# Optimization experiments

Hardware: AMD Instinct MI355X
Metric: run time of the kernel (lower is better)

Reference implementation:

```python
import jax, jax.numpy as jnp
import numpy as np

B, L, D, H, C = 16, 1024, 2048, 512, 2  # batch, doc_len, input_dim, hidden_dim, num_labels


def setup_inputs() -> dict:
    key = jax.random.key(0)
    ks = jax.random.split(key, 8)
    s_ih = 1.0 / np.sqrt(H)
    inp = {
        "x": jax.random.normal(ks[0], (B, L, D), dtype=jnp.float32),
        # PyTorch LSTM params (single layer, gate order i,f,g,o)
        "W_ih": jax.random.uniform(ks[1], (4 * H, D), minval=-s_ih, maxval=s_ih, dtype=jnp.float32),
        "W_hh": jax.random.uniform(ks[2], (4 * H, H), minval=-s_ih, maxval=s_ih, dtype=jnp.float32),
        "b_ih": jax.random.uniform(ks[3], (4 * H,), minval=-s_ih, maxval=s_ih, dtype=jnp.float32),
        "b_hh": jax.random.uniform(ks[4], (4 * H,), minval=-s_ih, maxval=s_ih, dtype=jnp.float32),
        # classifier linear
        "W_lin": jax.random.normal(ks[5], (C, H), dtype=jnp.float32) * 0.02,
        "b_lin": jnp.zeros((C,), dtype=jnp.float32),
        # attention gates, initialized as in the torch module
        "fwd_att": jnp.full((1, H), 0.001, dtype=jnp.float32),
        "bwd_att": jnp.full((1, H), 0.001, dtype=jnp.float32),
    }
    return inp


def _lstm(x, W_ih, W_hh, b_ih, b_hh):
    # x: [B, L, D] -> lstm_out: [B, L, H]
    b = b_ih + b_hh
    xg = jnp.einsum("bld,gd->blg", x, W_ih) + b  # precompute input projection [B,L,4H]

    def step(carry, xg_t):
        h, c = carry
        gates = xg_t + h @ W_hh.T
        i, f, g, o = jnp.split(gates, 4, axis=-1)
        i, f, o = jax.nn.sigmoid(i), jax.nn.sigmoid(f), jax.nn.sigmoid(o)
        g = jnp.tanh(g)
        c = f * c + i * g
        h = o * jnp.tanh(c)
        return (h, c), h

    h0 = jnp.zeros((x.shape[0], W_hh.shape[1]), dtype=x.dtype)
    _, hs = jax.lax.scan(step, (h0, h0), jnp.swapaxes(xg, 0, 1))
    return jnp.swapaxes(hs, 0, 1)  # [B, L, H]


def reference(x, W_ih, W_hh, b_ih, b_hh, W_lin, b_lin, fwd_att, bwd_att):
    lstm_out = _lstm(x, W_ih, W_hh, b_ih, b_hh)  # [B, L, H]
    # per-position gate: argmax of the linear classifier (same for fwd and bwd sums)
    logits = jnp.einsum("blh,ch->blc", lstm_out, W_lin) + b_lin  # [B, L, C]
    g = jnp.argmax(logits, axis=-1).astype(lstm_out.dtype)[..., None]  # [B, L, 1]
    term_f = g * lstm_out * fwd_att  # [B, L, H]
    term_b = g * lstm_out * bwd_att
    # forward_sum[i] = sum_{j<i} term_f[j]  (exclusive prefix sum)
    inc_f = jnp.cumsum(term_f, axis=1)
    cum_f = inc_f - term_f
    # backward_sum[i] = sum_{j>i} term_b[j]  (exclusive suffix sum)
    inc_b = jnp.cumsum(term_b, axis=1)
    cum_b = inc_b[:, -1:, :] - inc_b
    # fused = (lstm_out + cum_f) + (lstm_out + cum_b)
    return 2.0 * lstm_out + cum_f + cum_b
```

## Files before the change

### kernel.cpp

```cpp
#include <hip/hip_runtime.h>
#include <stdint.h>

typedef __bf16 bf16x8_t __attribute__((ext_vector_type(8)));
typedef float  f32x4_t  __attribute__((ext_vector_type(4)));

#define MFMA_BF16(A, Bv, C) __builtin_amdgcn_mfma_f32_16x16x32_bf16((A), (Bv), (C), 0, 0, 0)

static constexpr int BB = 16;
static constexpr int LL = 1024;
static constexpr int DD = 2048;
static constexpr int HH = 512;
static constexpr int GG = 4 * HH;
static constexpr int MM = BB * LL;

static constexpr size_t XBF_OFF   = 0;
static constexpr size_t WIHBF_OFF = XBF_OFF   + (size_t)MM * DD * 2;
static constexpr size_t WHHBF_OFF = WIHBF_OFF + (size_t)GG * DD * 2;
static constexpr size_t XGBF_OFF  = WHHBF_OFF + (size_t)GG * HH * 2;
static constexpr size_t GARR_OFF  = XGBF_OFF  + (size_t)MM * GG * 2;
static constexpr size_t PART_OFF  = GARR_OFF  + (size_t)MM * 4;
static constexpr size_t TBUF_OFF  = PART_OFF  + (size_t)BB * 8 * HH * 4;
static constexpr size_t WS_NEED   = TBUF_OFF  + (size_t)2 * BB * HH * 4;

__device__ __forceinline__ unsigned short f2bf(float f) {
  union { float f; uint32_t u; } v; v.f = f;
  uint32_t r = v.u + 0x7FFFu + ((v.u >> 16) & 1u);
  return (unsigned short)(r >> 16);
}
__device__ __forceinline__ float bf2f(unsigned short s) {
  union { uint32_t u; float f; } v; v.u = ((uint32_t)s) << 16;
  return v.f;
}
__device__ __forceinline__ float sigmoidf_fast(float x) { return 1.f / (1.f + __expf(-x)); }
__device__ __forceinline__ float tanhf_fast(float x) {
  float ax = fabsf(x);
  float e  = __expf(2.f * ax);
  float t  = 1.f - 2.f / (e + 1.f);
  return copysignf(t, x);
}
__device__ __forceinline__ void async_cp16(const void* g, void* lds) {
  __builtin_amdgcn_global_load_lds((const __attribute__((address_space(1))) uint32_t*)g,
                                   (__attribute__((address_space(3))) uint32_t*)lds, 16, 0, 0);
}

__global__ __launch_bounds__(256) void k_f32_to_bf16(const float* __restrict__ s,
                                                     unsigned short* __restrict__ d, int n4) {
  int i = blockIdx.x * 256 + threadIdx.x;
  int stride = gridDim.x * 256;
  for (; i < n4; i += stride) {
    float4 v = ((const float4*)s)[i];
    ushort4 o;
    o.x = f2bf(v.x); o.y = f2bf(v.y); o.z = f2bf(v.z); o.w = f2bf(v.w);
    ((ushort4*)d)[i] = o;
  }
}

__global__ __launch_bounds__(256) void k_gemm_xg(const unsigned short* __restrict__ A,
                                                 const unsigned short* __restrict__ Bw,
                                                 const float* __restrict__ b_ih,
                                                 const float* __restrict__ b_hh,
                                                 unsigned short* __restrict__ C) {
  __shared__ __align__(16) unsigned short As[128 * 32];
  __shared__ __align__(16) unsigned short Bs[128 * 32];
  const int bid = blockIdx.x;
  const int bn = bid & 15, bm = bid >> 4;
  const int row0 = bm * 128, col0 = bn * 128;
  const int tid = threadIdx.x;
  const int lane = tid & 63, w = tid >> 6;
  const int wr = w >> 1, wc = w & 1;
  const int l15 = lane & 15, l4 = lane >> 4;

  const f32x4_t z4 = {0.f, 0.f, 0.f, 0.f};
  f32x4_t acc[4][4];
#pragma unroll
  for (int mi = 0; mi < 4; ++mi)
#pragma unroll
    for (int ni = 0; ni < 4; ++ni) acc[mi][ni] = z4;

  const unsigned short* ga = A  + (size_t)(row0 + (tid >> 2)) * DD + (tid & 3) * 8;
  const unsigned short* gb = Bw + (size_t)(col0 + (tid >> 2)) * DD + (tid & 3) * 8;
  unsigned short* asw = As + w * 512;
  unsigned short* bsw = Bs + w * 512;

  for (int k0 = 0; k0 < DD; k0 += 32) {
    async_cp16(ga + k0,           asw);
    async_cp16(ga + k0 + 64 * DD, asw + 2048);
    async_cp16(gb + k0,           bsw);
    async_cp16(gb + k0 + 64 * DD, bsw + 2048);
    __syncthreads();
    bf16x8_t af[4], bfr[4];
#pragma unroll
    for (int mi = 0; mi < 4; ++mi)
      af[mi] = *(const bf16x8_t*)(As + (wr * 64 + mi * 16 + l15) * 32 + l4 * 8);
#pragma unroll
    for (int ni = 0; ni < 4; ++ni)
      bfr[ni] = *(const bf16x8_t*)(Bs + (wc * 64 + ni * 16 + l15) * 32 + l4 * 8);
#pragma unroll
    for (int mi = 0; mi < 4; ++mi)
#pragma unroll
      for (int ni = 0; ni < 4; ++ni)
        acc[mi][ni] = MFMA_BF16(af[mi], bfr[ni], acc[mi][ni]);
    __syncthreads();
  }
#pragma unroll
  for (int ni = 0; ni < 4; ++ni) {
    int col = col0 + wc * 64 + ni * 16 + l15;
    float bias = b_ih[col] + b_hh[col];
#pragma unroll
    for (int mi = 0; mi < 4; ++mi) {
      int rowb = row0 + wr * 64 + mi * 16 + l4 * 4;
#pragma unroll
      for (int r = 0; r < 4; ++r)
        C[(size_t)(rowb + r) * GG + col] = f2bf(acc[mi][ni][r] + bias);
    }
  }
}

__global__ __launch_bounds__(256) void k_lstm(const unsigned short* __restrict__ Whh,
                                              const unsigned short* __restrict__ xg,
                                              float* __restrict__ h_all,
                                              unsigned int* tbuf) {
  const int bid = blockIdx.x;
  const int b  = (bid & 7) + 8 * (bid >> 7);
  const int wg = (bid >> 3) & 15;
  const int tid = threadIdx.x;
  const int lane = tid & 63, w = tid >> 6;
  const int l15 = lane & 15, l4 = lane >> 4;
  const int K0 = wg * 32;

  __shared__ float gl[4][32];
  __shared__ __align__(16) unsigned short h_lds[HH];

  bf16x8_t wf[2][16];
#pragma unroll
  for (int mi = 0; mi < 2; ++mi) {
    const unsigned short* wrow = Whh + (size_t)(w * HH + K0 + mi * 16 + l15) * HH + l4 * 8;
#pragma unroll
    for (int kt = 0; kt < 16; ++kt)
      wf[mi][kt] = *(const bf16x8_t*)(wrow + kt * 32);
  }

  float c_reg = 0.f;
  const f32x4_t z4 = {0.f, 0.f, 0.f, 0.f};

  float xgi = 0.f, xgf = 0.f, xgc = 0.f, xgo = 0.f;
  const unsigned short* xr0 = xg + (size_t)(b << 10) * GG + K0 + (tid & 31);
  if (tid < 32) {
    xgi = bf2f(xr0[0]); xgf = bf2f(xr0[512]); xgc = bf2f(xr0[1024]); xgo = bf2f(xr0[1536]);
  }

  for (int t = 0; t < LL; ++t) {
    unsigned long long* src = (unsigned long long*)(tbuf + (((t & 1) * BB + b) << 9)) + tid;
    const unsigned int tg = (unsigned int)t;
    unsigned long long v;
    unsigned int guard = 0;
    for (;;) {
      v = __hip_atomic_load(src, __ATOMIC_RELAXED, __HIP_MEMORY_SCOPE_AGENT);
      if ((((unsigned int)(v >> 16) & 0xFFFFu) == tg) && ((unsigned int)(v >> 48) == tg)) break;
      if (++guard > (1u << 20)) break;
    }
    ushort2 hv2; hv2.x = (unsigned short)v; hv2.y = (unsigned short)(v >> 32);
    ((ushort2*)h_lds)[tid] = hv2;
    __syncthreads();

    f32x4_t acc0 = z4, acc1 = z4;
#pragma unroll
    for (int kt = 0; kt < 16; ++kt) {
      bf16x8_t hv = *(const bf16x8_t*)(h_lds + kt * 32 + l4 * 8);
      acc0 = MFMA_BF16(wf[0][kt], hv, acc0);
      acc1 = MFMA_BF16(wf[1][kt], hv, acc1);
    }
    if (l15 == 0) {
#pragma unroll
      for (int r = 0; r < 4; ++r) {
        gl[w][l4 * 4 + r]      = acc0[r];
        gl[w][16 + l4 * 4 + r] = acc1[r];
      }
    }
    __syncthreads();

    if (tid < 32) {
      float gi = sigmoidf_fast(gl[0][tid] + xgi);
      float gf = sigmoidf_fast(gl[1][tid] + xgf);
      float gc = tanhf_fast   (gl[2][tid] + xgc);
      float go = sigmoidf_fast(gl[3][tid] + xgo);
      c_reg = gf * c_reg + gi * gc;
      float h = go * tanhf_fast(c_reg);
      unsigned int word = ((unsigned int)(t + 1) << 16) | (unsigned int)f2bf(h);
      unsigned int* dst = tbuf + ((((t + 1) & 1) * BB + b) << 9) + K0 + tid;
      __hip_atomic_store(dst, word, __ATOMIC_RELAXED, __HIP_MEMORY_SCOPE_AGENT);
      h_all[(size_t)((b << 10) + t) * HH + K0 + tid] = h;
      if (t + 1 < LL) {
        const unsigned short* xr = xr0 + (size_t)(t + 1) * GG;
        xgi = bf2f(xr[0]); xgf = bf2f(xr[512]); xgc = bf2f(xr[1024]); xgo = bf2f(xr[1536]);
      }
    }
  }
}

__global__ __launch_bounds__(256) void k_gsel(const float* __restrict__ h, const float* __restrict__ Wlin,
                                              const float* __restrict__ blin, float* __restrict__ g) {
  const int lane = threadIdx.x & 63, w = threadIdx.x >> 6;
  const int idx = blockIdx.x * 4 + w;
  const float4* hp = (const float4*)(h + (size_t)idx * HH + lane * 8);
  const float4* w0 = (const float4*)(Wlin + lane * 8);
  const float4* w1 = (const float4*)(Wlin + HH + lane * 8);
  float4 h0 = hp[0], h1 = hp[1];
  float4 a0 = w0[0], a1 = w0[1], c0 = w1[0], c1 = w1[1];
  float s0 = h0.x*a0.x + h0.y*a0.y + h0.z*a0.z + h0.w*a0.w
           + h1.x*a1.x + h1.y*a1.y + h1.z*a1.z + h1.w*a1.w;
  float s1 = h0.x*c0.x + h0.y*c0.y + h0.z*c0.z + h0.w*c0.w
           + h1.x*c1.x + h1.y*c1.y + h1.z*c1.z + h1.w*c1.w;
#pragma unroll
  for (int off = 32; off > 0; off >>= 1) {
    s0 += __shfl_xor(s0, off);
    s1 += __shfl_xor(s1, off);
  }
  if (lane == 0) g[idx] = (s1 + blin[1] > s0 + blin[0]) ? 1.f : 0.f;
}

__global__ __launch_bounds__(256) void k_scan_a(const float* __restrict__ h, const float* __restrict__ g,
                                                float* __restrict__ part) {
  const int bid = blockIdx.x;
  const int b = bid >> 4, seg = (bid >> 1) & 7, kc = bid & 1;
  const int k = kc * 256 + threadIdx.x;
  __shared__ float gs[128];
  if (threadIdx.x < 128) gs[threadIdx.x] = g[b * LL + seg * 128 + threadIdx.x];
  __syncthreads();
  const float* hp = h + ((size_t)(b * LL + seg * 128)) * HH + k;
  float sum = 0.f;
#pragma unroll 4
  for (int l = 0; l < 128; ++l) sum += gs[l] * hp[(size_t)l * HH];
  part[(b * 8 + seg) * HH + k] = sum;
}

__global__ __launch_bounds__(256) void k_scan_b(float* __restrict__ h, const float* __restrict__ g,
                                                const float* __restrict__ part,
                                                const float* __restrict__ fwd, const float* __restrict__ bwd) {
  const int bid = blockIdx.x;
  const int b = bid >> 4, seg = (bid >> 1) & 7, kc = bid & 1;
  const int k = kc * 256 + threadIdx.x;
  __shared__ float gs[128];
  if (threadIdx.x < 128) gs[threadIdx.x] = g[b * LL + seg * 128 + threadIdx.x];
  __syncthreads();
  float base = 0.f, total = 0.f;
#pragma unroll
  for (int s = 0; s < 8; ++s) {
    float v = part[(b * 8 + s) * HH + k];
    total += v;
    if (s < seg) base += v;
  }
  const float fa = fwd[k], ba = bwd[k];
  float run = base;
  float* hp = h + ((size_t)(b * LL + seg * 128)) * HH + k;
  for (int l = 0; l < 128; ++l) {
    float hv = hp[(size_t)l * HH];
    float term = gs[l] * hv;
    hp[(size_t)l * HH] = 2.f * hv + fa * run + ba * (total - run - term);
    run += term;
  }
}

extern "C" void kernel_launch(void* const* d_in, const int* in_sizes, int n_in,
                              void* d_out, int out_size, void* d_ws, size_t ws_size,
                              hipStream_t stream) {
  if (ws_size < WS_NEED) return;
  const float* x    = (const float*)d_in[0];
  const float* Wih  = (const float*)d_in[1];
  const float* Whh  = (const float*)d_in[2];
  const float* b_ih = (const float*)d_in[3];
  const float* b_hh = (const float*)d_in[4];
  const float* Wlin = (const float*)d_in[5];
  const float* blin = (const float*)d_in[6];
  const float* fwd  = (const float*)d_in[7];
  const float* bwd  = (const float*)d_in[8];
  char* ws = (char*)d_ws;
  unsigned short* xbf   = (unsigned short*)(ws + XBF_OFF);
  unsigned short* wihbf = (unsigned short*)(ws + WIHBF_OFF);
  unsigned short* whhbf = (unsigned short*)(ws + WHHBF_OFF);
  unsigned short* xgbf  = (unsigned short*)(ws + XGBF_OFF);
  float*          garr  = (float*)(ws + GARR_OFF);
  float*          part  = (float*)(ws + PART_OFF);
  unsigned int*   tbuf  = (unsigned int*)(ws + TBUF_OFF);
  float* out = (float*)d_out;

  (void)hipMemsetAsync(ws + TBUF_OFF, 0, (size_t)2 * BB * HH * 4, stream);

  k_f32_to_bf16<<<2048, 256, 0, stream>>>(x,   xbf,   MM * DD / 4);
  k_f32_to_bf16<<<1024, 256, 0, stream>>>(Wih, wihbf, GG * DD / 4);
  k_f32_to_bf16<<<256,  256, 0, stream>>>(Whh, whhbf, GG * HH / 4);
  k_gemm_xg<<<(MM / 128) * (GG / 128), 256, 0, stream>>>(xbf, wihbf, b_ih, b_hh, xgbf);
  k_lstm<<<256, 256, 0, stream>>>(whhbf, xgbf, out, tbuf);
  k_gsel<<<MM / 4, 256, 0, stream>>>(out, Wlin, blin, garr);
  k_scan_a<<<256, 256, 0, stream>>>(out, garr, part);
  k_scan_b<<<256, 256, 0, stream>>>(out, garr, part, fwd, bwd);
}
```

Before: 1.616 ms.

## Distribute gate activations across waves and prefetch input projections in LSTM recurrence

Moves the xg add and the sigmoid/tanh gate activations from a single 32-thread section into the four waves, each applying its own gate right after the MFMA. The next timestep's xg values are now issued before the spin-wait, so their latency hides behind the barrier. The poll loop keeps two atomic loads in flight, and the MFMA chain is split into two independent accumulators to shorten the dependency. This trims the serial critical path per timestep, at the cost of more registers and extra loads in every wave.

```diff
diff --git a/kernel.cpp b/kernel.cpp
--- a/kernel.cpp
+++ b/kernel.cpp
@@ -116,10 +116,10 @@
   }
 }
 
-__global__ __launch_bounds__(256) void k_lstm(const unsigned short* __restrict__ Whh,
-                                              const unsigned short* __restrict__ xg,
-                                              float* __restrict__ h_all,
-                                              unsigned int* tbuf) {
+__global__ __launch_bounds__(256, 1) void k_lstm(const unsigned short* __restrict__ Whh,
+                                                 const unsigned short* __restrict__ xg,
+                                                 float* __restrict__ h_all,
+                                                 unsigned int* tbuf) {
   const int bid = blockIdx.x;
   const int b  = (bid & 7) + 8 * (bid >> 7);
   const int wg = (bid >> 3) & 15;
@@ -143,58 +143,73 @@
   float c_reg = 0.f;
   const f32x4_t z4 = {0.f, 0.f, 0.f, 0.f};
 
-  float xgi = 0.f, xgf = 0.f, xgc = 0.f, xgo = 0.f;
-  const unsigned short* xr0 = xg + (size_t)(b << 10) * GG + K0 + (tid & 31);
-  if (tid < 32) {
-    xgi = bf2f(xr0[0]); xgf = bf2f(xr0[512]); xgc = bf2f(xr0[1024]); xgo = bf2f(xr0[1536]);
+  const unsigned short* xgw = xg + (size_t)(b << 10) * GG + w * HH + K0 + l4 * 4;
+  float xfa[4], xfb[4];
+  {
+    ushort4 ua = *(const ushort4*)xgw;
+    ushort4 ub = *(const ushort4*)(xgw + 16);
+    xfa[0] = bf2f(ua.x); xfa[1] = bf2f(ua.y); xfa[2] = bf2f(ua.z); xfa[3] = bf2f(ua.w);
+    xfb[0] = bf2f(ub.x); xfb[1] = bf2f(ub.y); xfb[2] = bf2f(ub.z); xfb[3] = bf2f(ub.w);
   }
 
   for (int t = 0; t < LL; ++t) {
+    const int tn = (t + 1 < LL) ? t + 1 : t;
+    ushort4 ua = *(const ushort4*)(xgw + (size_t)tn * GG);
+    ushort4 ub = *(const ushort4*)(xgw + (size_t)tn * GG + 16);
+
     unsigned long long* src = (unsigned long long*)(tbuf + (((t & 1) * BB + b) << 9)) + tid;
-    const unsigned int tg = (unsigned int)t;
+    const unsigned long long tg = (unsigned long long)(unsigned int)t;
     unsigned long long v;
-    unsigned int guard = 0;
-    for (;;) {
-      v = __hip_atomic_load(src, __ATOMIC_RELAXED, __HIP_MEMORY_SCOPE_AGENT);
-      if ((((unsigned int)(v >> 16) & 0xFFFFu) == tg) && ((unsigned int)(v >> 48) == tg)) break;
-      if (++guard > (1u << 20)) break;
+    {
+      unsigned long long p0 = __hip_atomic_load(src, __ATOMIC_RELAXED, __HIP_MEMORY_SCOPE_AGENT);
+      unsigned long long p1 = __hip_atomic_load(src, __ATOMIC_RELAXED, __HIP_MEMORY_SCOPE_AGENT);
+      unsigned int guard = 0;
+      for (;;) {
+        if ((((p0 >> 16) & 0xFFFFull) == tg) && ((p0 >> 48) == tg)) { v = p0; break; }
+        p0 = p1;
+        p1 = __hip_atomic_load(src, __ATOMIC_RELAXED, __HIP_MEMORY_SCOPE_AGENT);
+        if (++guard > (1u << 20)) { v = p0; break; }
+      }
     }
     ushort2 hv2; hv2.x = (unsigned short)v; hv2.y = (unsigned short)(v >> 32);
     ((ushort2*)h_lds)[tid] = hv2;
     __syncthreads();
 
-    f32x4_t acc0 = z4, acc1 = z4;
-#pragma unroll
-    for (int kt = 0; kt < 16; ++kt) {
-      bf16x8_t hv = *(const bf16x8_t*)(h_lds + kt * 32 + l4 * 8);
-      acc0 = MFMA_BF16(wf[0][kt], hv, acc0);
-      acc1 = MFMA_BF16(wf[1][kt], hv, acc1);
-    }
+    f32x4_t a0a = z4, a0b = z4, a1a = z4, a1b = z4;
+#pragma unroll
+    for (int kt = 0; kt < 8; ++kt) {
+      bf16x8_t hva = *(const bf16x8_t*)(h_lds + kt * 32 + l4 * 8);
+      bf16x8_t hvb = *(const bf16x8_t*)(h_lds + (kt + 8) * 32 + l4 * 8);
+      a0a = MFMA_BF16(wf[0][kt],     hva, a0a);
+      a1a = MFMA_BF16(wf[1][kt],     hva, a1a);
+      a0b = MFMA_BF16(wf[0][kt + 8], hvb, a0b);
+      a1b = MFMA_BF16(wf[1][kt + 8], hvb, a1b);
+    }
+
     if (l15 == 0) {
+      f32x4_t acc0 = a0a + a0b, acc1 = a1a + a1b;
 #pragma unroll
       for (int r = 0; r < 4; ++r) {
-        gl[w][l4 * 4 + r]      = acc0[r];
-        gl[w][16 + l4 * 4 + r] = acc1[r];
+        float g0 = acc0[r] + xfa[r];
+        float g1 = acc1[r] + xfb[r];
+        gl[w][l4 * 4 + r]      = (w == 2) ? tanhf_fast(g0) : sigmoidf_fast(g0);
+        gl[w][16 + l4 * 4 + r] = (w == 2) ? tanhf_fast(g1) : sigmoidf_fast(g1);
       }
     }
     __syncthreads();
 
     if (tid < 32) {
-      float gi = sigmoidf_fast(gl[0][tid] + xgi);
-      float gf = sigmoidf_fast(gl[1][tid] + xgf);
-      float gc = tanhf_fast   (gl[2][tid] + xgc);
-      float go = sigmoidf_fast(gl[3][tid] + xgo);
+      float gi = gl[0][tid], gf = gl[1][tid], gc = gl[2][tid], go = gl[3][tid];
       c_reg = gf * c_reg + gi * gc;
       float h = go * tanhf_fast(c_reg);
       unsigned int word = ((unsigned int)(t + 1) << 16) | (unsigned int)f2bf(h);
       unsigned int* dst = tbuf + ((((t + 1) & 1) * BB + b) << 9) + K0 + tid;
       __hip_atomic_store(dst, word, __ATOMIC_RELAXED, __HIP_MEMORY_SCOPE_AGENT);
       h_all[(size_t)((b << 10) + t) * HH + K0 + tid] = h;
-      if (t + 1 < LL) {
-        const unsigned short* xr = xr0 + (size_t)(t + 1) * GG;
-        xgi = bf2f(xr[0]); xgf = bf2f(xr[512]); xgc = bf2f(xr[1024]); xgo = bf2f(xr[1536]);
-      }
-    }
+    }
+
+    xfa[0] = bf2f(ua.x); xfa[1] = bf2f(ua.y); xfa[2] = bf2f(ua.z); xfa[3] = bf2f(ua.w);
+    xfb[0] = bf2f(ub.x); xfb[1] = bf2f(ub.y); xfb[2] = bf2f(ub.z); xfb[3] = bf2f(ub.w);
   }
 }
 
```

Result: slower. 2.280 ms (+41.1%).

## Restructure LSTM recurrence to batch all sequences per block with split-K MFMA

Applied to the files above, without the earlier changes.

The recurrent kernel now runs 16 blocks of 1024 threads, each owning 32 hidden units for all 16 batch rows, instead of 256 blocks each handling one batch row. Each block uses the batch as the MFMA N dimension and splits K across four wave groups, reducing partial sums through LDS. Gate nonlinearities are spread across all threads, and the next step's input projection is prefetched. The intent is to cut the number of cross-block sync participants and to use the matrix units on a full 16-wide batch tile. In exchange it adds an extra LDS reduction stage and a wider polling read of the shared h buffer.

```diff
diff --git a/kernel.cpp b/kernel.cpp
--- a/kernel.cpp
+++ b/kernel.cpp
@@ -116,85 +116,125 @@
   }
 }
 
-__global__ __launch_bounds__(256) void k_lstm(const unsigned short* __restrict__ Whh,
-                                              const unsigned short* __restrict__ xg,
-                                              float* __restrict__ h_all,
-                                              unsigned int* tbuf) {
-  const int bid = blockIdx.x;
-  const int b  = (bid & 7) + 8 * (bid >> 7);
-  const int wg = (bid >> 3) & 15;
+__global__ __launch_bounds__(1024, 1) void k_lstm(const unsigned short* __restrict__ Whh,
+                                                  const unsigned short* __restrict__ xg,
+                                                  float* __restrict__ h_all,
+                                                  unsigned int* tbuf) {
+  const int wg = blockIdx.x;
+  const int S0 = wg * 32;
   const int tid = threadIdx.x;
-  const int lane = tid & 63, w = tid >> 6;
+  const int lane = tid & 63;
+  const int wid = tid >> 6;
+  const int g  = wid & 3;
+  const int kp = wid >> 2;
   const int l15 = lane & 15, l4 = lane >> 4;
-  const int K0 = wg * 32;
-
-  __shared__ float gl[4][32];
-  __shared__ __align__(16) unsigned short h_lds[HH];
-
-  bf16x8_t wf[2][16];
-#pragma unroll
-  for (int mi = 0; mi < 2; ++mi) {
-    const unsigned short* wrow = Whh + (size_t)(w * HH + K0 + mi * 16 + l15) * HH + l4 * 8;
-#pragma unroll
-    for (int kt = 0; kt < 16; ++kt)
-      wf[mi][kt] = *(const bf16x8_t*)(wrow + kt * 32);
-  }
-
+
+  __shared__ __align__(16) unsigned short Hb[16][536];
+  __shared__ float part[16][2][4][64];
+  __shared__ float gl[4][32][17];
+
+  f32x4_t wa[2][4];
+#pragma unroll
+  for (int tile = 0; tile < 2; ++tile) {
+    const unsigned short* wrow = Whh + (size_t)(g * HH + S0 + tile * 16 + l15) * HH + kp * 128 + l4 * 8;
+#pragma unroll
+    for (int kc = 0; kc < 4; ++kc)
+      wa[tile][kc] = *(const f32x4_t*)(wrow + kc * 32);
+  }
+#pragma unroll
+  for (int tile = 0; tile < 2; ++tile)
+#pragma unroll
+    for (int kc = 0; kc < 4; ++kc)
+      asm volatile("" : "+v"(wa[tile][kc]));
+
+  const int b_r = tid & 15;
+  const int rh = (tid >> 4) & 1;
+  const int q  = (tid >> 5) & 3;
+  const int tile_r = (tid >> 7) & 1;
+  const int g_r = tid >> 8;
+  const int j_r = tile_r * 16 + q * 4 + rh * 2;
+  const uint32_t* xgp32 = (const uint32_t*)(xg + (size_t)(b_r << 10) * GG + g_r * HH + S0 + j_r);
+
+  const int b_t = tid >> 5, j_t = tid & 31;
   float c_reg = 0.f;
+
   const f32x4_t z4 = {0.f, 0.f, 0.f, 0.f};
-
-  float xgi = 0.f, xgf = 0.f, xgc = 0.f, xgo = 0.f;
-  const unsigned short* xr0 = xg + (size_t)(b << 10) * GG + K0 + (tid & 31);
-  if (tid < 32) {
-    xgi = bf2f(xr0[0]); xgf = bf2f(xr0[512]); xgc = bf2f(xr0[1024]); xgo = bf2f(xr0[1536]);
-  }
+  uint32_t xcur = xgp32[0];
 
   for (int t = 0; t < LL; ++t) {
-    unsigned long long* src = (unsigned long long*)(tbuf + (((t & 1) * BB + b) << 9)) + tid;
-    const unsigned int tg = (unsigned int)t;
-    unsigned long long v;
+    unsigned long long* src = (unsigned long long*)(tbuf + ((t & 1) << 13)) + tid * 4;
+    const unsigned long long msk = 0xFFFF0000FFFF0000ull;
+    const unsigned long long expv = ((unsigned long long)(unsigned int)t << 16)
+                                  | ((unsigned long long)(unsigned int)t << 48);
+    unsigned long long v0, v1, v2, v3;
     unsigned int guard = 0;
     for (;;) {
-      v = __hip_atomic_load(src, __ATOMIC_RELAXED, __HIP_MEMORY_SCOPE_AGENT);
-      if ((((unsigned int)(v >> 16) & 0xFFFFu) == tg) && ((unsigned int)(v >> 48) == tg)) break;
+      v0 = __hip_atomic_load(src + 0, __ATOMIC_RELAXED, __HIP_MEMORY_SCOPE_AGENT);
+      v1 = __hip_atomic_load(src + 1, __ATOMIC_RELAXED, __HIP_MEMORY_SCOPE_AGENT);
+      v2 = __hip_atomic_load(src + 2, __ATOMIC_RELAXED, __HIP_MEMORY_SCOPE_AGENT);
+      v3 = __hip_atomic_load(src + 3, __ATOMIC_RELAXED, __HIP_MEMORY_SCOPE_AGENT);
+      if (((v0 & msk) == expv) && ((v1 & msk) == expv) &&
+          ((v2 & msk) == expv) && ((v3 & msk) == expv)) break;
       if (++guard > (1u << 20)) break;
     }
-    ushort2 hv2; hv2.x = (unsigned short)v; hv2.y = (unsigned short)(v >> 32);
-    ((ushort2*)h_lds)[tid] = hv2;
-    __syncthreads();
+    {
+      uint4 d;
+      d.x = (uint32_t)(v0 & 0xFFFFu) | ((uint32_t)(v0 >> 16) & 0xFFFF0000u);
+      d.y = (uint32_t)(v1 & 0xFFFFu) | ((uint32_t)(v1 >> 16) & 0xFFFF0000u);
+      d.z = (uint32_t)(v2 & 0xFFFFu) | ((uint32_t)(v2 >> 16) & 0xFFFF0000u);
+      d.w = (uint32_t)(v3 & 0xFFFFu) | ((uint32_t)(v3 >> 16) & 0xFFFF0000u);
+      *(uint4*)&Hb[tid >> 6][(tid & 63) * 8] = d;
+    }
+    __syncthreads();
+
+    uint32_t xnx = 0;
+    if (t + 1 < LL) xnx = xgp32[(size_t)(t + 1) * (GG / 2)];
 
     f32x4_t acc0 = z4, acc1 = z4;
 #pragma unroll
-    for (int kt = 0; kt < 16; ++kt) {
-      bf16x8_t hv = *(const bf16x8_t*)(h_lds + kt * 32 + l4 * 8);
-      acc0 = MFMA_BF16(wf[0][kt], hv, acc0);
-      acc1 = MFMA_BF16(wf[1][kt], hv, acc1);
-    }
-    if (l15 == 0) {
-#pragma unroll
-      for (int r = 0; r < 4; ++r) {
-        gl[w][l4 * 4 + r]      = acc0[r];
-        gl[w][16 + l4 * 4 + r] = acc1[r];
+    for (int kc = 0; kc < 4; ++kc) {
+      bf16x8_t hb = *(const bf16x8_t*)&Hb[l15][kp * 128 + kc * 32 + l4 * 8];
+      acc0 = MFMA_BF16(__builtin_bit_cast(bf16x8_t, wa[0][kc]), hb, acc0);
+      acc1 = MFMA_BF16(__builtin_bit_cast(bf16x8_t, wa[1][kc]), hb, acc1);
+    }
+#pragma unroll
+    for (int r = 0; r < 4; ++r) {
+      part[wid][0][r][lane] = acc0[r];
+      part[wid][1][r][lane] = acc1[r];
+    }
+    __syncthreads();
+
+    {
+      const int li = q * 16 + b_r;
+      const int r0 = rh * 2;
+      float s0 = 0.f, s1 = 0.f;
+#pragma unroll
+      for (int kk = 0; kk < 4; ++kk) {
+        s0 += part[kk * 4 + g_r][tile_r][r0][li];
+        s1 += part[kk * 4 + g_r][tile_r][r0 + 1][li];
       }
-    }
-    __syncthreads();
-
-    if (tid < 32) {
-      float gi = sigmoidf_fast(gl[0][tid] + xgi);
-      float gf = sigmoidf_fast(gl[1][tid] + xgf);
-      float gc = tanhf_fast   (gl[2][tid] + xgc);
-      float go = sigmoidf_fast(gl[3][tid] + xgo);
+      s0 += bf2f((unsigned short)(xcur & 0xFFFFu));
+      s1 += bf2f((unsigned short)(xcur >> 16));
+      float a0, a1;
+      if (g_r == 2) { a0 = tanhf_fast(s0);    a1 = tanhf_fast(s1); }
+      else          { a0 = sigmoidf_fast(s0); a1 = sigmoidf_fast(s1); }
+      gl[g_r][j_r][b_r]     = a0;
+      gl[g_r][j_r + 1][b_r] = a1;
+    }
+    __syncthreads();
+
+    if (tid < 512) {
+      float gi = gl[0][j_t][b_t], gf = gl[1][j_t][b_t];
+      float gc = gl[2][j_t][b_t], go = gl[3][j_t][b_t];
       c_reg = gf * c_reg + gi * gc;
       float h = go * tanhf_fast(c_reg);
       unsigned int word = ((unsigned int)(t + 1) << 16) | (unsigned int)f2bf(h);
-      unsigned int* dst = tbuf + ((((t + 1) & 1) * BB + b) << 9) + K0 + tid;
+      unsigned int* dst = tbuf + (((t + 1) & 1) << 13) + (b_t << 9) + S0 + j_t;
       __hip_atomic_store(dst, word, __ATOMIC_RELAXED, __HIP_MEMORY_SCOPE_AGENT);
-      h_all[(size_t)((b << 10) + t) * HH + K0 + tid] = h;
-      if (t + 1 < LL) {
-        const unsigned short* xr = xr0 + (size_t)(t + 1) * GG;
-        xgi = bf2f(xr[0]); xgf = bf2f(xr[512]); xgc = bf2f(xr[1024]); xgo = bf2f(xr[1536]);
-      }
-    }
+      h_all[(size_t)((b_t << 10) + t) * HH + S0 + j_t] = h;
+    }
+
+    xcur = xnx;
   }
 }
 
@@ -290,7 +330,7 @@
   k_f32_to_bf16<<<1024, 256, 0, stream>>>(Wih, wihbf, GG * DD / 4);
   k_f32_to_bf16<<<256,  256, 0, stream>>>(Whh, whhbf, GG * HH / 4);
   k_gemm_xg<<<(MM / 128) * (GG / 128), 256, 0, stream>>>(xbf, wihbf, b_ih, b_hh, xgbf);
-  k_lstm<<<256, 256, 0, stream>>>(whhbf, xgbf, out, tbuf);
+  k_lstm<<<16, 1024, 0, stream>>>(whhbf, xgbf, out, tbuf);
   k_gsel<<<MM / 4, 256, 0, stream>>>(out, Wlin, blin, garr);
   k_scan_a<<<256, 256, 0, stream>>>(out, garr, part);
   k_scan_b<<<256, 256, 0, stream>>>(out, garr, part, fwd, bwd);
```

After: 3.306 ms. 105% more time.
